# Performance work log

Hardware: AMD Instinct MI355X
Metric: run time of the kernel (lower is better)

## Reference

```python
import jax, jax.numpy as jnp
import numpy as np

NUM_EXPERTS = 8
HIDDEN = 2048
EXPERT_DIM = 2048  # intermediate_size per shard (tp_size=1)
TOTAL_TOKENS = 32768  # divisible by NUM_EXPERTS


def setup_inputs() -> dict:
    key = jax.random.key(0)
    k1, k2, k3 = jax.random.split(key, 3)
    hidden_states = jax.random.normal(k1, (TOTAL_TOKENS, HIDDEN), dtype=jnp.float32)
    # (E, H, 2*D): gate and up projections concatenated on last dim
    gate_up_proj = jax.random.normal(k2, (NUM_EXPERTS, HIDDEN, 2 * EXPERT_DIM), dtype=jnp.float32) * 0.02
    # (E, D, H)
    down_proj = jax.random.normal(k3, (NUM_EXPERTS, EXPERT_DIM, HIDDEN), dtype=jnp.float32) * 0.02
    return {"hidden_states": hidden_states, "gate_up_proj": gate_up_proj, "down_proj": down_proj}


def reference(hidden_states, gate_up_proj, down_proj):
    E, H = gate_up_proj.shape[0], gate_up_proj.shape[1]
    # tokens are pre-sorted per expert: (E, T, H)
    x = hidden_states.reshape(E, -1, H)
    # grouped GEMM: (E,T,H) @ (E,H,2D) -> (E,T,2D)
    gate_up = jnp.einsum('eth,ehd->etd', x, gate_up_proj)
    gate, up = jnp.split(gate_up, 2, axis=-1)
    # SwiGLU epilogue then down projection: (E,T,D) @ (E,D,H) -> (E,T,H)
    act = up * jax.nn.silu(gate)
    out = jnp.einsum('etd,edh->eth', act, down_proj)
    # tp_size=1 -> all_reduce is identity
    return out.reshape(-1, H)
```

## Files before the change

kernel.cpp:

```cpp
#include <hip/hip_runtime.h>


#define E_EXPERTS 8
#define TPE 4096
#define KD 2048

typedef __bf16 bf16_t;
typedef __bf16 bf16x4 __attribute__((ext_vector_type(4)));
typedef __bf16 bf16x8 __attribute__((ext_vector_type(8)));
typedef float f32x4 __attribute__((ext_vector_type(4)));

#define GLOAD16(src, dst)                                               \
  __builtin_amdgcn_global_load_lds(                                     \
      (const __attribute__((address_space(1))) void*)(src),             \
      (__attribute__((address_space(3))) void*)(dst), 16, 0, 0)

__global__ void cvt_f32_bf16_kernel(const float* __restrict__ in,
                                    bf16_t* __restrict__ out, long n4) {
  long i = (long)blockIdx.x * blockDim.x + threadIdx.x;
  const long stride = (long)gridDim.x * blockDim.x;
  const float4* in4 = (const float4*)in;
  bf16x4* out4 = (bf16x4*)out;
  for (; i < n4; i += stride) {
    float4 v = in4[i];
    bf16x4 o = {(bf16_t)v.x, (bf16_t)v.y, (bf16_t)v.z, (bf16_t)v.w};
    out4[i] = o;
  }
}

__global__ void transpose_cvt_kernel(const float* __restrict__ W,
                                     bf16_t* __restrict__ WT, int K, int N) {
  __shared__ float tile[64][65];
  const int e = blockIdx.z;
  const float* Wp = W + (size_t)e * K * N;
  bf16_t* Tp = WT + (size_t)e * N * K;
  const int n0 = blockIdx.x * 64, k0 = blockIdx.y * 64;
  const int rr = threadIdx.x >> 4;
  const int cc = (threadIdx.x & 15) * 4;
#pragma unroll
  for (int p = 0; p < 4; ++p) {
    const int k = rr + p * 16;
    float4 v = *(const float4*)(Wp + (size_t)(k0 + k) * N + n0 + cc);
    tile[k][cc + 0] = v.x;
    tile[k][cc + 1] = v.y;
    tile[k][cc + 2] = v.z;
    tile[k][cc + 3] = v.w;
  }
  __syncthreads();
#pragma unroll
  for (int p = 0; p < 4; ++p) {
    const int n = rr + p * 16;
    bf16x4 o;
#pragma unroll
    for (int j = 0; j < 4; ++j) o[j] = (bf16_t)tile[cc + j][n];
    *(bf16x4*)(Tp + (size_t)(n0 + n) * K + k0 + cc) = o;
  }
}

template <bool FUSED, int NTN>
__global__ __launch_bounds__(512, 4) void moe_gemm_tlp_kernel(
    const bf16_t* __restrict__ A, const bf16_t* __restrict__ Bm,
    void* __restrict__ Cout) {
  constexpr int NT = KD / 32;

  __shared__ alignas(16) bf16_t As[3][64][64];
  __shared__ alignas(16) bf16_t Bs[3][128][64];

  const int NWG = gridDim.x;
  int wg = blockIdx.x;
  wg = (wg & 7) * (NWG >> 3) + (wg >> 3);
  const int e = wg / (32 * NTN);
  const int rem = wg % (32 * NTN);
  const int mt = rem / NTN, ntile = rem % NTN;
  const int t0 = mt * 128, n0 = ntile * 256;

  const int tid = threadIdx.x;
  const int wid = tid >> 6, lane = tid & 63;
  const int wr = wid >> 2, wc = wid & 3;

  const bf16_t* Ae = A + (size_t)e * TPE * KD + (size_t)t0 * KD;
  const bf16_t* Be = Bm + (size_t)e * (size_t)(FUSED ? 4096 : 2048) * KD;

  const int sp = lane >> 3;
  const int lc = lane & 7;

  const int pA = wid * 8 + sp;
  const int cA = lc ^ (pA & 7);
  const bf16_t* aSrc = Ae + (size_t)(pA + 64 * (cA >> 2)) * KD + (cA & 3) * 8;

  const bf16_t* bSrc[2];
#pragma unroll
  for (int i = 0; i < 2; ++i) {
    const int p = wid * 16 + i * 8 + sp;
    const int c = lc ^ (p & 7);
    const int R = n0 + p + 128 * (c >> 2);
    int srow;
    if constexpr (FUSED)
      srow = ((R >> 5) << 4) + (R & 15) + ((R >> 4) & 1) * 2048;
    else
      srow = R;
    bSrc[i] = Be + (size_t)srow * KD + (c & 3) * 8;
  }

  auto stageA = [&](int kt, int slot) {
    const int k0 = (kt & (NT - 1)) * 32;
    GLOAD16(aSrc + k0, &As[slot][wid * 8][0]);
  };
  auto stageB = [&](int kt, int slot) {
    const int k0 = (kt & (NT - 1)) * 32;
#pragma unroll
    for (int i = 0; i < 2; ++i)
      GLOAD16(bSrc[i] + k0, &Bs[slot][wid * 16 + i * 8][0]);
  };

  const int la = lane & 15, kg4 = lane >> 4;

  f32x4 acc[4][4] = {};
  bf16x8 am[4];
  bf16x8 bn[2];

  auto readA = [&](int slot) {
#pragma unroll
    for (int m = 0; m < 4; ++m) {
      const int r = wr * 64 + m * 16 + la;
      const int p = r & 63, h = r >> 6;
      const int c = (h * 4 + kg4) ^ (p & 7);
      am[m] = *(const bf16x8*)&As[slot][p][c * 8];
    }
  };
  auto readB = [&](int slot, int q) {
#pragma unroll
    for (int j = 0; j < 2; ++j) {
      const int R = wc * 64 + q * 32 + j * 16 + la;
      const int p = R & 127, h = R >> 7;
      const int c = (h * 4 + kg4) ^ (p & 7);
      bn[j] = *(const bf16x8*)&Bs[slot][p][c * 8];
    }
  };

#define W0 asm volatile("s_waitcnt lgkmcnt(0)" ::: "memory")
#define VMC3 asm volatile("s_waitcnt vmcnt(3)" ::: "memory")
#define BAR __builtin_amdgcn_s_barrier()
#define SCHED0 __builtin_amdgcn_sched_barrier(0)
#define PRIO1 __builtin_amdgcn_s_setprio(1)
#define PRIO0 __builtin_amdgcn_s_setprio(0)

  stageA(0, 0); stageB(0, 0);
  stageA(1, 1); stageB(1, 1);
  VMC3;
  BAR; SCHED0;

  int s = 0, s2 = 2;
  for (int t = 0; t < NT; ++t) {
    readA(s);
    readB(s, 0);
    stageA(t + 2, s2);
    stageB(t + 2, s2);
    W0; SCHED0;
    PRIO1;
#pragma unroll
    for (int m = 0; m < 4; ++m) {
      acc[m][0] = __builtin_amdgcn_mfma_f32_16x16x32_bf16(am[m], bn[0],
                                                          acc[m][0], 0, 0, 0);
      acc[m][1] = __builtin_amdgcn_mfma_f32_16x16x32_bf16(am[m], bn[1],
                                                          acc[m][1], 0, 0, 0);
    }
    PRIO0;
    readB(s, 1);
    W0; SCHED0;
    PRIO1;
#pragma unroll
    for (int m = 0; m < 4; ++m) {
      acc[m][2] = __builtin_amdgcn_mfma_f32_16x16x32_bf16(am[m], bn[0],
                                                          acc[m][2], 0, 0, 0);
      acc[m][3] = __builtin_amdgcn_mfma_f32_16x16x32_bf16(am[m], bn[1],
                                                          acc[m][3], 0, 0, 0);
    }
    PRIO0;
    VMC3;
    BAR; SCHED0;
    s = (s == 2) ? 0 : s + 1;
    s2 = (s2 == 2) ? 0 : s2 + 1;
  }

  const int rbase = t0 + wr * 64;
  if constexpr (FUSED) {
    bf16_t* Cp = (bf16_t*)Cout + (size_t)e * TPE * KD;
    const int jb = (n0 >> 1) + 32 * wc;
#pragma unroll
    for (int m = 0; m < 4; ++m)
#pragma unroll
      for (int q = 0; q < 2; ++q)
#pragma unroll
        for (int r = 0; r < 4; ++r) {
          const int row = rbase + m * 16 + kg4 * 4 + r;
          const int col = jb + q * 16 + la;
          const float g = acc[m][2 * q][r], u = acc[m][2 * q + 1][r];
          const float sg = 1.0f / (1.0f + __expf(-g));
          Cp[(size_t)row * KD + col] = (bf16_t)(u * g * sg);
        }
  } else {
    float* Cp = (float*)Cout + (size_t)e * TPE * KD;
#pragma unroll
    for (int m = 0; m < 4; ++m)
#pragma unroll
      for (int n = 0; n < 4; ++n)
#pragma unroll
        for (int r = 0; r < 4; ++r) {
          const int row = rbase + m * 16 + kg4 * 4 + r;
          const int col = n0 + wc * 64 + n * 16 + la;
          Cp[(size_t)row * KD + col] = acc[m][n][r];
        }
  }
#undef W0
#undef VMC3
#undef BAR
#undef SCHED0
#undef PRIO1
#undef PRIO0
}

extern "C" void kernel_launch(void* const* d_in, const int* in_sizes, int n_in,
                              void* d_out, int out_size, void* d_ws,
                              size_t ws_size, hipStream_t stream) {
  const float* hs = (const float*)d_in[0];
  const float* w1 = (const float*)d_in[1];
  const float* w2 = (const float*)d_in[2];

  char* ws = (char*)d_ws;
  bf16_t* xb = (bf16_t*)(ws);
  bf16_t* w1t = (bf16_t*)(ws + (size_t)134217728);
  bf16_t* w2t = (bf16_t*)(ws + (size_t)268435456);
  bf16_t* act = (bf16_t*)(ws + (size_t)335544320);

  const long n4 = (long)E_EXPERTS * TPE * KD / 4;
  cvt_f32_bf16_kernel<<<2048, 256, 0, stream>>>(hs, xb, n4);
  transpose_cvt_kernel<<<dim3(64, 32, 8), 256, 0, stream>>>(w1, w1t, 2048, 4096);
  transpose_cvt_kernel<<<dim3(32, 32, 8), 256, 0, stream>>>(w2, w2t, 2048, 2048);
  moe_gemm_tlp_kernel<true, 16><<<4096, 512, 0, stream>>>(xb, w1t, (void*)act);
  moe_gemm_tlp_kernel<false, 8><<<2048, 512, 0, stream>>>(act, w2t, d_out);
}
```

Baseline: 1.069 ms.

## Fuse down-proj weight transpose into gate-up GEMM grid and unroll K loop

The gate-up GEMM launch doubles its grid. Half the workgroups, interleaved in groups of eight, perform the down-projection weight transpose and convert to bf16, which removes a separate kernel launch and lets that memory-bound work overlap the compute-bound GEMM. The K loop is also unrolled by three with constant LDS slot offsets and precomputed read pointers, which removes the slot-rotation arithmetic. The risk is that the transpose blocks compete with GEMM blocks for occupancy and bandwidth, and they use LDS sized for the GEMM.

```diff
diff --git a/kernel.cpp b/kernel.cpp
--- a/kernel.cpp
+++ b/kernel.cpp
@@ -57,18 +57,65 @@
   }
 }
 
-template <bool FUSED, int NTN>
+__device__ inline void tw2_transpose(const float* __restrict__ W,
+                                     bf16_t* __restrict__ WT, int b,
+                                     void* lds) {
+  float(*tile)[65] = (float(*)[65])lds;
+#pragma unroll 1
+  for (int jj = 0; jj < 2; ++jj) {
+    const int job = b + jj * 4096;
+    const int nx = job & 31, ky = (job >> 5) & 31, e = job >> 10;
+    const float* Wp = W + (size_t)e * KD * KD;
+    bf16_t* Tp = WT + (size_t)e * KD * KD;
+    const int n0 = nx * 64, k0 = ky * 64;
+    const int rr = threadIdx.x >> 4;
+    const int cc = (threadIdx.x & 15) * 4;
+    if (jj) __syncthreads();
+#pragma unroll
+    for (int p = 0; p < 2; ++p) {
+      const int k = rr + p * 32;
+      float4 v = *(const float4*)(Wp + (size_t)(k0 + k) * KD + n0 + cc);
+      tile[k][cc + 0] = v.x;
+      tile[k][cc + 1] = v.y;
+      tile[k][cc + 2] = v.z;
+      tile[k][cc + 3] = v.w;
+    }
+    __syncthreads();
+#pragma unroll
+    for (int p = 0; p < 2; ++p) {
+      const int n = rr + p * 32;
+      bf16x4 o;
+#pragma unroll
+      for (int q = 0; q < 4; ++q) o[q] = (bf16_t)tile[cc + q][n];
+      *(bf16x4*)(Tp + (size_t)(n0 + n) * KD + k0 + cc) = o;
+    }
+  }
+}
+
+template <bool FUSED, int NTN, bool TW2>
 __global__ __launch_bounds__(512, 4) void moe_gemm_tlp_kernel(
     const bf16_t* __restrict__ A, const bf16_t* __restrict__ Bm,
-    void* __restrict__ Cout) {
+    void* __restrict__ Cout, const float* __restrict__ W2src,
+    bf16_t* __restrict__ W2dst) {
   constexpr int NT = KD / 32;
 
   __shared__ alignas(16) bf16_t As[3][64][64];
   __shared__ alignas(16) bf16_t Bs[3][128][64];
 
-  const int NWG = gridDim.x;
-  int wg = blockIdx.x;
-  wg = (wg & 7) * (NWG >> 3) + (wg >> 3);
+  int j;
+  if constexpr (TW2) {
+    const int x = blockIdx.x & 15, g = blockIdx.x >> 4;
+    if (x >= 8) {
+      tw2_transpose(W2src, W2dst, 8 * g + (x - 8), (void*)&As[0][0][0]);
+      return;
+    }
+    j = 8 * g + x;
+  } else {
+    j = blockIdx.x;
+  }
+
+  const int NWG = TW2 ? (gridDim.x >> 1) : gridDim.x;
+  int wg = (j & 7) * (NWG >> 3) + (j >> 3);
   const int e = wg / (32 * NTN);
   const int rem = wg % (32 * NTN);
   const int mt = rem / NTN, ntile = rem % NTN;
@@ -84,9 +131,9 @@
   const int sp = lane >> 3;
   const int lc = lane & 7;
 
-  const int pA = wid * 8 + sp;
-  const int cA = lc ^ (pA & 7);
-  const bf16_t* aSrc = Ae + (size_t)(pA + 64 * (cA >> 2)) * KD + (cA & 3) * 8;
+  const int pAr = wid * 8 + sp;
+  const int cAr = lc ^ (pAr & 7);
+  const bf16_t* aSrc = Ae + (size_t)(pAr + 64 * (cAr >> 2)) * KD + (cAr & 3) * 8;
 
   const bf16_t* bSrc[2];
 #pragma unroll
@@ -115,28 +162,28 @@
 
   const int la = lane & 15, kg4 = lane >> 4;
 
+  const bf16_t* pA[4];
+#pragma unroll
+  for (int m = 0; m < 4; ++m) {
+    const int r = wr * 64 + m * 16 + la;
+    const int p = r & 63, h = r >> 6;
+    const int c = (h * 4 + kg4) ^ (p & 7);
+    pA[m] = &As[0][p][c * 8];
+  }
+  const bf16_t* pB[4];
+#pragma unroll
+  for (int q = 0; q < 2; ++q)
+#pragma unroll
+    for (int jf = 0; jf < 2; ++jf) {
+      const int R = wc * 64 + q * 32 + jf * 16 + la;
+      const int p = R & 127, h = R >> 7;
+      const int c = (h * 4 + kg4) ^ (p & 7);
+      pB[q * 2 + jf] = &Bs[0][p][c * 8];
+    }
+
   f32x4 acc[4][4] = {};
   bf16x8 am[4];
   bf16x8 bn[2];
-
-  auto readA = [&](int slot) {
-#pragma unroll
-    for (int m = 0; m < 4; ++m) {
-      const int r = wr * 64 + m * 16 + la;
-      const int p = r & 63, h = r >> 6;
-      const int c = (h * 4 + kg4) ^ (p & 7);
-      am[m] = *(const bf16x8*)&As[slot][p][c * 8];
-    }
-  };
-  auto readB = [&](int slot, int q) {
-#pragma unroll
-    for (int j = 0; j < 2; ++j) {
-      const int R = wc * 64 + q * 32 + j * 16 + la;
-      const int p = R & 127, h = R >> 7;
-      const int c = (h * 4 + kg4) ^ (p & 7);
-      bn[j] = *(const bf16x8*)&Bs[slot][p][c * 8];
-    }
-  };
 
 #define W0 asm volatile("s_waitcnt lgkmcnt(0)" ::: "memory")
 #define VMC3 asm volatile("s_waitcnt vmcnt(3)" ::: "memory")
@@ -145,43 +192,52 @@
 #define PRIO1 __builtin_amdgcn_s_setprio(1)
 #define PRIO0 __builtin_amdgcn_s_setprio(0)
 
+#define TILE(t, S, S2)                                                       \
+  do {                                                                       \
+    am[0] = *(const bf16x8*)(pA[0] + (S) * 4096);                            \
+    am[1] = *(const bf16x8*)(pA[1] + (S) * 4096);                            \
+    am[2] = *(const bf16x8*)(pA[2] + (S) * 4096);                            \
+    am[3] = *(const bf16x8*)(pA[3] + (S) * 4096);                            \
+    bn[0] = *(const bf16x8*)(pB[0] + (S) * 8192);                            \
+    bn[1] = *(const bf16x8*)(pB[1] + (S) * 8192);                            \
+    stageA((t) + 2, S2);                                                     \
+    stageB((t) + 2, S2);                                                     \
+    W0; SCHED0;                                                              \
+    PRIO1;                                                                   \
+    _Pragma("unroll") for (int m = 0; m < 4; ++m) {                          \
+      acc[m][0] = __builtin_amdgcn_mfma_f32_16x16x32_bf16(am[m], bn[0],      \
+                                                          acc[m][0], 0, 0, 0); \
+      acc[m][1] = __builtin_amdgcn_mfma_f32_16x16x32_bf16(am[m], bn[1],      \
+                                                          acc[m][1], 0, 0, 0); \
+    }                                                                        \
+    PRIO0;                                                                   \
+    bn[0] = *(const bf16x8*)(pB[2] + (S) * 8192);                            \
+    bn[1] = *(const bf16x8*)(pB[3] + (S) * 8192);                            \
+    W0; SCHED0;                                                              \
+    PRIO1;                                                                   \
+    _Pragma("unroll") for (int m = 0; m < 4; ++m) {                          \
+      acc[m][2] = __builtin_amdgcn_mfma_f32_16x16x32_bf16(am[m], bn[0],      \
+                                                          acc[m][2], 0, 0, 0); \
+      acc[m][3] = __builtin_amdgcn_mfma_f32_16x16x32_bf16(am[m], bn[1],      \
+                                                          acc[m][3], 0, 0, 0); \
+    }                                                                        \
+    PRIO0;                                                                   \
+    VMC3;                                                                    \
+    BAR; SCHED0;                                                             \
+  } while (0)
+
   stageA(0, 0); stageB(0, 0);
   stageA(1, 1); stageB(1, 1);
   VMC3;
   BAR; SCHED0;
 
-  int s = 0, s2 = 2;
-  for (int t = 0; t < NT; ++t) {
-    readA(s);
-    readB(s, 0);
-    stageA(t + 2, s2);
-    stageB(t + 2, s2);
-    W0; SCHED0;
-    PRIO1;
-#pragma unroll
-    for (int m = 0; m < 4; ++m) {
-      acc[m][0] = __builtin_amdgcn_mfma_f32_16x16x32_bf16(am[m], bn[0],
-                                                          acc[m][0], 0, 0, 0);
-      acc[m][1] = __builtin_amdgcn_mfma_f32_16x16x32_bf16(am[m], bn[1],
-                                                          acc[m][1], 0, 0, 0);
-    }
-    PRIO0;
-    readB(s, 1);
-    W0; SCHED0;
-    PRIO1;
-#pragma unroll
-    for (int m = 0; m < 4; ++m) {
-      acc[m][2] = __builtin_amdgcn_mfma_f32_16x16x32_bf16(am[m], bn[0],
-                                                          acc[m][2], 0, 0, 0);
-      acc[m][3] = __builtin_amdgcn_mfma_f32_16x16x32_bf16(am[m], bn[1],
-                                                          acc[m][3], 0, 0, 0);
-    }
-    PRIO0;
-    VMC3;
-    BAR; SCHED0;
-    s = (s == 2) ? 0 : s + 1;
-    s2 = (s2 == 2) ? 0 : s2 + 1;
-  }
+  int t = 0;
+  for (; t < NT - 3; t += 3) {
+    TILE(t, 0, 2);
+    TILE(t + 1, 1, 0);
+    TILE(t + 2, 2, 1);
+  }
+  TILE(t, 0, 2);
 
   const int rbase = t0 + wr * 64;
   if constexpr (FUSED) {
@@ -218,6 +274,7 @@
 #undef SCHED0
 #undef PRIO1
 #undef PRIO0
+#undef TILE
 }
 
 extern "C" void kernel_launch(void* const* d_in, const int* in_sizes, int n_in,
@@ -236,7 +293,8 @@
   const long n4 = (long)E_EXPERTS * TPE * KD / 4;
   cvt_f32_bf16_kernel<<<2048, 256, 0, stream>>>(hs, xb, n4);
   transpose_cvt_kernel<<<dim3(64, 32, 8), 256, 0, stream>>>(w1, w1t, 2048, 4096);
-  transpose_cvt_kernel<<<dim3(32, 32, 8), 256, 0, stream>>>(w2, w2t, 2048, 2048);
-  moe_gemm_tlp_kernel<true, 16><<<4096, 512, 0, stream>>>(xb, w1t, (void*)act);
-  moe_gemm_tlp_kernel<false, 8><<<2048, 512, 0, stream>>>(act, w2t, d_out);
-}
+  moe_gemm_tlp_kernel<true, 16, true>
+      <<<8192, 512, 0, stream>>>(xb, w1t, (void*)act, w2, w2t);
+  moe_gemm_tlp_kernel<false, 8, false>
+      <<<2048, 512, 0, stream>>>(act, w2t, d_out, nullptr, nullptr);
+}
```

New measurement: 1.532 ms. +43.3%, slower.
